# Performance work log

Measured on AMD Instinct MI355X. Metric: run time of the kernel, lower is better.

Reference implementation:

```python
import jax, jax.numpy as jnp
import numpy as np

_BN_EPS = 1e-5
_BN_SCALE = 1.0 / np.sqrt(1.0 + _BN_EPS)  # eval-mode BN with running_mean=0, running_var=1


def _bn(x, g, b):
    # eval-mode BatchNorm1d over channel dim (last axis here)
    return x * (g * _BN_SCALE) + b


def _sa_layer(src_xyz, dst_xyz, cur_i, idx, empty, p_w, p_g, p_b, m_w, m_g, m_b):
    # src_xyz: (N,3), dst_xyz: (M,3), cur_i: (N,D), idx: (M,S) int, empty: (M,) bool
    idx = idx.astype(jnp.int32)
    sp = src_xyz[idx]                       # (M,S,3) neighbor gather
    dp = dst_xyz[:, None, :]                # (M,1,3)
    feat6 = jnp.concatenate([sp - dp, jnp.broadcast_to(dp, sp.shape)], axis=-1)  # (M,S,6)
    off = jax.nn.silu(_bn(jnp.einsum('msc,dc->msd', feat6, p_w), p_g, p_b))      # (M,S,D)
    x = off + cur_i[idx]                    # (M,S,D)
    x = jnp.where(empty[:, None, None], 0.0, x)
    h = jax.nn.relu(_bn(jnp.einsum('msd,hd->msh', x, m_w), m_g, m_b))            # (M,S,H)
    return jnp.max(h, axis=1)               # (M,H) max-pool over neighbors


def reference(src_xyz, src_feats, dst_xyz, idx0, idx1, empty0, empty1,
              fc0_w, fc0_b, p0_w, p0_g, p0_b, m0_w, m0_g, m0_b,
              fc1_w, fc1_b, p1_w, p1_g, p1_b, m1_w, m1_g, m1_b,
              out_w, out_g, out_b):
    cur0 = src_feats @ fc0_w.T + fc0_b      # (N,64) fc_i of layer 0
    cur1 = src_feats @ fc1_w.T + fc1_b      # (N,64) fc_i of layer 1
    f0 = _sa_layer(src_xyz, dst_xyz, cur0, idx0, empty0, p0_w, p0_g, p0_b, m0_w, m0_g, m0_b)
    f1 = _sa_layer(src_xyz, dst_xyz, cur1, idx1, empty1, p1_w, p1_g, p1_b, m1_w, m1_g, m1_b)
    feats = jnp.concatenate([f0, f1], axis=1)                                    # (M,256)
    out = jax.nn.relu(_bn(feats @ out_w.T, out_g, out_b))                        # out_conv (1x1 conv)
    return out                               # (M,256)


def setup_inputs() -> dict:
    key = jax.random.key(0)
    ks = jax.random.split(key, 24)
    N, M, Cin, D, H, S0, S1 = 65536, 16384, 64, 64, 128, 16, 32
    inp = {
        'src_xyz': jax.random.normal(ks[0], (N, 3), jnp.float32) * 20.0,
        'src_feats': jax.random.normal(ks[1], (N, Cin), jnp.float32),
        'dst_xyz': jax.random.normal(ks[2], (M, 3), jnp.float32) * 20.0,
        'idx0': jax.random.randint(ks[3], (M, S0), 0, N, jnp.int32),
        'idx1': jax.random.randint(ks[4], (M, S1), 0, N, jnp.int32),
        'empty0': jax.random.bernoulli(ks[5], 0.05, (M,)),
        'empty1': jax.random.bernoulli(ks[6], 0.05, (M,)),
        'fc0_w': jax.random.normal(ks[7], (D, Cin), jnp.float32) / np.sqrt(Cin),
        'fc0_b': jnp.zeros((D,), jnp.float32),
        'p0_w': jax.random.normal(ks[8], (D, 6), jnp.float32) / np.sqrt(6.0),
        'p0_g': jnp.ones((D,), jnp.float32),
        'p0_b': jnp.zeros((D,), jnp.float32),
        'm0_w': jax.random.normal(ks[9], (H, D), jnp.float32) / np.sqrt(D),
        'm0_g': jnp.ones((H,), jnp.float32),
        'm0_b': jnp.zeros((H,), jnp.float32),
        'fc1_w': jax.random.normal(ks[10], (D, Cin), jnp.float32) / np.sqrt(Cin),
        'fc1_b': jnp.zeros((D,), jnp.float32),
        'p1_w': jax.random.normal(ks[11], (D, 6), jnp.float32) / np.sqrt(6.0),
        'p1_g': jnp.ones((D,), jnp.float32),
        'p1_b': jnp.zeros((D,), jnp.float32),
        'm1_w': jax.random.normal(ks[12], (H, D), jnp.float32) / np.sqrt(D),
        'm1_g': jnp.ones((H,), jnp.float32),
        'm1_b': jnp.zeros((H,), jnp.float32),
        'out_w': jax.random.normal(ks[13], (256, 2 * H), jnp.float32) / np.sqrt(2.0 * H),
        'out_g': jnp.ones((256,), jnp.float32),
        'out_b': jnp.zeros((256,), jnp.float32),
    }
    return inp
```

## Files before the change

kernel.cpp:

```cpp
#include <hip/hip_runtime.h>
#include <hip/hip_bf16.h>

typedef unsigned short ushort_t;
typedef unsigned int uint_t;
typedef __attribute__((ext_vector_type(8))) short v8s;
typedef __attribute__((ext_vector_type(4))) float v4f;

#define BN_SCALE 0.9999950000374997f

__device__ __forceinline__ float bf2f(ushort_t u) {
    union { uint_t i; float f; } v;
    v.i = ((uint_t)u) << 16;
    return v.f;
}
__device__ __forceinline__ ushort_t f2bf(float f) {
    union { uint_t i; float f; } v;
    v.f = f;
    uint_t b = v.i;
    b += 0x7fffu + ((b >> 16) & 1u);
    return (ushort_t)(b >> 16);
}

__device__ __forceinline__ v8s cvt8(const float* __restrict__ p) {
    v8s f;
    #pragma unroll
    for (int j = 0; j < 8; ++j) f[j] = (short)f2bf(p[j]);
    return f;
}

__global__ __launch_bounds__(256) void convw_kernel(
    const float* __restrict__ w, ushort_t* __restrict__ wb)
{
    const int i = (blockIdx.x * 256 + threadIdx.x) * 4;
    const v4f v = *(const v4f*)(w + i);
    ushort_t r0 = f2bf(v[0]), r1 = f2bf(v[1]), r2 = f2bf(v[2]), r3 = f2bf(v[3]);
    uint_t lo = (uint_t)r0 | ((uint_t)r1 << 16);
    uint_t hi = (uint_t)r2 | ((uint_t)r3 << 16);
    *(uint2*)(wb + i) = make_uint2(lo, hi);
}

__global__ __launch_bounds__(256) void cur_kernel(
    const float* __restrict__ src_feats,
    const float* __restrict__ fc0_w, const float* __restrict__ fc0_b,
    const float* __restrict__ fc1_w, const float* __restrict__ fc1_b,
    ushort_t* __restrict__ cur0, ushort_t* __restrict__ cur1)
{
    const int tid  = threadIdx.x;
    const int lane = tid & 63;
    const int wid  = tid >> 6;
    const int col  = lane & 15;
    const int quad = lane >> 4;
    const int row0 = blockIdx.x * 64 + wid * 16;

    v8s afrag[2];
    #pragma unroll
    for (int kf = 0; kf < 2; ++kf)
        afrag[kf] = cvt8(src_feats + (size_t)(row0 + col) * 64 + kf * 32 + quad * 8);

    v4f acc[8];
    v8s bfrag[8][2];
    #pragma unroll
    for (int ct = 0; ct < 8; ++ct) {
        const int d = (ct & 3) * 16 + col;
        const float* w = (ct < 4 ? fc0_w : fc1_w) + d * 64;
        const float  b = (ct < 4 ? fc0_b : fc1_b)[d];
        acc[ct] = (v4f){b, b, b, b};
        #pragma unroll
        for (int kf = 0; kf < 2; ++kf)
            bfrag[ct][kf] = cvt8(w + kf * 32 + quad * 8);
    }

    #pragma unroll
    for (int kf = 0; kf < 2; ++kf)
        #pragma unroll
        for (int ct = 0; ct < 8; ++ct)
            acc[ct] = __builtin_amdgcn_mfma_f32_16x16x32_bf16(
                afrag[kf], bfrag[ct][kf], acc[ct], 0, 0, 0);

    #pragma unroll
    for (int ct = 0; ct < 8; ++ct) {
        ushort_t* dst = (ct < 4) ? cur0 : cur1;
        const int d = (ct & 3) * 16 + col;
        #pragma unroll
        for (int r = 0; r < 4; ++r) {
            const int n = row0 + quad * 4 + r;
            dst[(size_t)n * 64 + d] = f2bf(acc[ct][r]);
        }
    }
}

template <int S>
__device__ __forceinline__ void sa_body(
    const int bid,
    const float* __restrict__ src_xyz,
    const float* __restrict__ dst_xyz,
    const int*   __restrict__ idx,
    const int*   __restrict__ empty,
    const float* __restrict__ p_w,
    const float* __restrict__ p_g,
    const float* __restrict__ p_b,
    const float* __restrict__ m_w,
    const float* __restrict__ m_g,
    const float* __restrict__ m_b,
    const ushort_t* __restrict__ cur,
    ushort_t*    __restrict__ f01,
    const int layer_off,
    ushort_t* xlds,
    v4f*      flds)
{
    constexpr int PAIRS = 128;
    constexpr int MB = PAIRS / S;
    constexpr int XP = 72;
    constexpr int T  = S / 4;

    const int tid  = threadIdx.x;
    const int lane = tid & 63;
    const int wid  = tid >> 6;
    const int m0   = bid * MB;

    {
        const int p  = tid >> 1;
        const int hf = tid & 1;
        const int m  = m0 + p / S;
        const int i  = idx[(size_t)m * S + (p & (S - 1))];
        const uint_t* crow = (const uint_t*)(cur + (size_t)i * 64) + hf * 16;
        const uint4 c0 = *(const uint4*)(crow + 0);
        const uint4 c1 = *(const uint4*)(crow + 4);
        const uint4 c2 = *(const uint4*)(crow + 8);
        const uint4 c3 = *(const uint4*)(crow + 12);
        uint_t* drow = (uint_t*)(xlds + p * XP) + hf * 16;
        *(uint4*)(drow + 0)  = c0;
        *(uint4*)(drow + 4)  = c1;
        *(uint4*)(drow + 8)  = c2;
        *(uint4*)(drow + 12) = c3;
    }
    if (tid < PAIRS) {
        const int p = tid;
        const int m = m0 + p / S;
        const int i = idx[(size_t)m * S + (p & (S - 1))];
        const float dx = dst_xyz[m * 3 + 0];
        const float dy = dst_xyz[m * 3 + 1];
        const float dz = dst_xyz[m * 3 + 2];
        v4f r;
        r[0] = src_xyz[i * 3 + 0] - dx;
        r[1] = src_xyz[i * 3 + 1] - dy;
        r[2] = src_xyz[i * 3 + 2] - dz;
        r[3] = 0.0f;
        flds[p] = r;
    }

    const int dd = (lane & 31) * 2;
    const int psub = lane >> 5;
    const float pgA = p_g[dd] * BN_SCALE;
    const float pgB = p_g[dd + 1] * BN_SCALE;
    const float pbA = p_b[dd];
    const float pbB = p_b[dd + 1];
    const float pwA0 = p_w[dd * 6 + 0] * pgA;
    const float pwA1 = p_w[dd * 6 + 1] * pgA;
    const float pwA2 = p_w[dd * 6 + 2] * pgA;
    const float pdA0 = p_w[dd * 6 + 3] * pgA;
    const float pdA1 = p_w[dd * 6 + 4] * pgA;
    const float pdA2 = p_w[dd * 6 + 5] * pgA;
    const float pwB0 = p_w[dd * 6 + 6] * pgB;
    const float pwB1 = p_w[dd * 6 + 7] * pgB;
    const float pwB2 = p_w[dd * 6 + 8] * pgB;
    const float pdB0 = p_w[dd * 6 + 9] * pgB;
    const float pdB1 = p_w[dd * 6 + 10] * pgB;
    const float pdB2 = p_w[dd * 6 + 11] * pgB;

    __syncthreads();

    const int tbase = wid * T;
    #pragma unroll
    for (int mi = 0; mi < MB; ++mi) {
        const int m = m0 + mi;
        const float dx = dst_xyz[m * 3 + 0];
        const float dy = dst_xyz[m * 3 + 1];
        const float dz = dst_xyz[m * 3 + 2];
        const int   em = empty[m];
        const float vbA = fmaf(pdA0, dx, fmaf(pdA1, dy, fmaf(pdA2, dz, pbA)));
        const float vbB = fmaf(pdB0, dx, fmaf(pdB1, dy, fmaf(pdB2, dz, pbB)));

        #pragma unroll
        for (int it = 0; it < T / 2; ++it) {
            const int p = mi * S + tbase + it * 2 + psub;
            const v4f r = flds[p];
            const uint_t cu = *(const uint_t*)(xlds + p * XP + dd);
            const float c0 = __uint_as_float(cu << 16);
            const float c1 = __uint_as_float(cu & 0xffff0000u);

            const float v0 = fmaf(pwA0, r[0], fmaf(pwA1, r[1], fmaf(pwA2, r[2], vbA)));
            const float v1 = fmaf(pwB0, r[0], fmaf(pwB1, r[1], fmaf(pwB2, r[2], vbB)));
            const float rc0 = __builtin_amdgcn_rcpf(1.0f + __expf(-v0));
            const float rc1 = __builtin_amdgcn_rcpf(1.0f + __expf(-v1));
            float x0 = fmaf(v0, rc0, c0);
            float x1 = fmaf(v1, rc1, c1);
            x0 = em ? 0.0f : x0;
            x1 = em ? 0.0f : x1;

            float2 f2; f2.x = x0; f2.y = x1;
            union { __hip_bfloat162 h2; uint_t u; } pk;
            pk.h2 = __float22bfloat162_rn(f2);
            *(uint_t*)(xlds + p * XP + dd) = pk.u;
        }
    }

    const int col  = lane & 15;
    const int quad = lane >> 4;
    v8s bfrag[2][2];
    float mgv[2], mbv[2];
    #pragma unroll
    for (int c = 0; c < 2; ++c) {
        const int h = (wid * 2 + c) * 16 + col;
        #pragma unroll
        for (int kf = 0; kf < 2; ++kf)
            bfrag[c][kf] = cvt8(m_w + h * 64 + kf * 32 + quad * 8);
        mgv[c] = m_g[h] * BN_SCALE;
        mbv[c] = m_b[h];
    }

    __syncthreads();

    #pragma unroll
    for (int mi = 0; mi < MB; ++mi) {
        const int m = m0 + mi;
        v4f acc[S / 16][2];
        #pragma unroll
        for (int rt = 0; rt < S / 16; ++rt)
            #pragma unroll
            for (int c = 0; c < 2; ++c)
                acc[rt][c] = (v4f)0.0f;

        #pragma unroll
        for (int rt = 0; rt < S / 16; ++rt) {
            #pragma unroll
            for (int kf = 0; kf < 2; ++kf) {
                const v8s afrag = *(const v8s*)(
                    xlds + ((mi * S + rt * 16 + col)) * XP + kf * 32 + quad * 8);
                acc[rt][0] = __builtin_amdgcn_mfma_f32_16x16x32_bf16(
                    afrag, bfrag[0][kf], acc[rt][0], 0, 0, 0);
                acc[rt][1] = __builtin_amdgcn_mfma_f32_16x16x32_bf16(
                    afrag, bfrag[1][kf], acc[rt][1], 0, 0, 0);
            }
        }

        float vmax0 = 0.0f, vmax1 = 0.0f;
        #pragma unroll
        for (int c = 0; c < 2; ++c) {
            float vm = 0.0f;
            #pragma unroll
            for (int rt = 0; rt < S / 16; ++rt)
                #pragma unroll
                for (int r = 0; r < 4; ++r) {
                    const float y = fmaf(acc[rt][c][r], mgv[c], mbv[c]);
                    vm = fmaxf(vm, y);
                }
            vm = fmaxf(vm, __shfl_xor(vm, 16));
            vm = fmaxf(vm, __shfl_xor(vm, 32));
            if (c == 0) vmax0 = vm; else vmax1 = vm;
        }
        if (lane < 32) {
            const int c = lane >> 4;
            const float val = (c == 0) ? vmax0 : vmax1;
            f01[m * 256 + layer_off + (wid * 2 + c) * 16 + (lane & 15)] = f2bf(val);
        }
    }
}

__global__ __launch_bounds__(256, 6) void sa_fused_kernel(
    const float* __restrict__ src_xyz, const float* __restrict__ dst_xyz,
    const int* __restrict__ idx0, const int* __restrict__ empty0,
    const float* __restrict__ p0_w, const float* __restrict__ p0_g, const float* __restrict__ p0_b,
    const float* __restrict__ m0_w, const float* __restrict__ m0_g, const float* __restrict__ m0_b,
    const ushort_t* __restrict__ cur0,
    const int* __restrict__ idx1, const int* __restrict__ empty1,
    const float* __restrict__ p1_w, const float* __restrict__ p1_g, const float* __restrict__ p1_b,
    const float* __restrict__ m1_w, const float* __restrict__ m1_g, const float* __restrict__ m1_b,
    const ushort_t* __restrict__ cur1,
    ushort_t* __restrict__ f01, const int G32)
{
    __shared__ ushort_t xlds[128 * 72];
    __shared__ v4f      flds[128];

    const int b = blockIdx.x;
    if (b < G32)
        sa_body<32>(b, src_xyz, dst_xyz, idx1, empty1, p1_w, p1_g, p1_b,
                    m1_w, m1_g, m1_b, cur1, f01, 128, xlds, flds);
    else
        sa_body<16>(b - G32, src_xyz, dst_xyz, idx0, empty0, p0_w, p0_g, p0_b,
                    m0_w, m0_g, m0_b, cur0, f01, 0, xlds, flds);
}

__global__ __launch_bounds__(256) void out_kernel(
    const ushort_t* __restrict__ f01,
    const ushort_t* __restrict__ out_wb,
    const float*    __restrict__ out_g,
    const float*    __restrict__ out_b,
    float*          __restrict__ out)
{
    const int tid  = threadIdx.x;
    const int lane = tid & 63;
    const int wid  = tid >> 6;
    const int col  = lane & 15;
    const int quad = lane >> 4;
    const int m0   = blockIdx.x * 16;

    v8s afrag[8];
    #pragma unroll
    for (int kf = 0; kf < 8; ++kf)
        afrag[kf] = *(const v8s*)(f01 + (size_t)(m0 + col) * 256 + kf * 32 + quad * 8);

    v4f acc[4];
    #pragma unroll
    for (int c = 0; c < 4; ++c) acc[c] = (v4f)0.0f;

    #pragma unroll
    for (int kf = 0; kf < 8; ++kf) {
        #pragma unroll
        for (int c = 0; c < 4; ++c) {
            const int n = (wid * 4 + c) * 16 + col;
            const v8s b = *(const v8s*)(out_wb + (size_t)n * 256 + kf * 32 + quad * 8);
            acc[c] = __builtin_amdgcn_mfma_f32_16x16x32_bf16(afrag[kf], b, acc[c], 0, 0, 0);
        }
    }

    #pragma unroll
    for (int c = 0; c < 4; ++c) {
        const int n  = (wid * 4 + c) * 16 + col;
        const float og = out_g[n] * BN_SCALE;
        const float ob = out_b[n];
        #pragma unroll
        for (int r = 0; r < 4; ++r) {
            float y = fmaf(acc[c][r], og, ob);
            y = fmaxf(y, 0.0f);
            out[(size_t)(m0 + quad * 4 + r) * 256 + n] = y;
        }
    }
}

extern "C" void kernel_launch(void* const* d_in, const int* in_sizes, int n_in,
                              void* d_out, int out_size, void* d_ws, size_t ws_size,
                              hipStream_t stream)
{
    const float* src_xyz   = (const float*)d_in[0];
    const float* src_feats = (const float*)d_in[1];
    const float* dst_xyz   = (const float*)d_in[2];
    const int*   idx0      = (const int*)d_in[3];
    const int*   idx1      = (const int*)d_in[4];
    const int*   empty0    = (const int*)d_in[5];
    const int*   empty1    = (const int*)d_in[6];
    const float* fc0_w     = (const float*)d_in[7];
    const float* fc0_b     = (const float*)d_in[8];
    const float* p0_w      = (const float*)d_in[9];
    const float* p0_g      = (const float*)d_in[10];
    const float* p0_b      = (const float*)d_in[11];
    const float* m0_w      = (const float*)d_in[12];
    const float* m0_g      = (const float*)d_in[13];
    const float* m0_b      = (const float*)d_in[14];
    const float* fc1_w     = (const float*)d_in[15];
    const float* fc1_b     = (const float*)d_in[16];
    const float* p1_w      = (const float*)d_in[17];
    const float* p1_g      = (const float*)d_in[18];
    const float* p1_b      = (const float*)d_in[19];
    const float* m1_w      = (const float*)d_in[20];
    const float* m1_g      = (const float*)d_in[21];
    const float* m1_b      = (const float*)d_in[22];
    const float* out_w     = (const float*)d_in[23];
    const float* out_g     = (const float*)d_in[24];
    const float* out_b     = (const float*)d_in[25];

    const int N = in_sizes[0] / 3;
    const int M = in_sizes[2] / 3;

    ushort_t* cur0   = (ushort_t*)d_ws;
    ushort_t* cur1   = cur0 + (size_t)N * 64;
    ushort_t* f01    = cur1 + (size_t)N * 64;
    ushort_t* out_wb = f01 + (size_t)M * 256;

    const int G32 = M / 4;
    const int G16 = M / 8;

    convw_kernel<<<64, 256, 0, stream>>>(out_w, out_wb);
    cur_kernel<<<N / 64, 256, 0, stream>>>(src_feats, fc0_w, fc0_b, fc1_w, fc1_b,
                                           cur0, cur1);
    sa_fused_kernel<<<G32 + G16, 256, 0, stream>>>(
        src_xyz, dst_xyz,
        idx0, empty0, p0_w, p0_g, p0_b, m0_w, m0_g, m0_b, cur0,
        idx1, empty1, p1_w, p1_g, p1_b, m1_w, m1_g, m1_b, cur1,
        f01, G32);
    out_kernel<<<M / 16, 256, 0, stream>>>(f01, out_wb, out_g, out_b,
                                           (float*)d_out);
}
```

Baseline: 202.6 us.

## Split MLP work by neighbor-group per wave and pre-convert m_w to bf16

The MFMA stage changes from each wave handling 32 output channels for every centroid to each wave owning whole centroids and computing all 128 channels. A-fragments are loaded from LDS once per centroid and reused across 8 channel tiles. B-fragments now come from a bf16 weight copy produced by extra convw launches instead of per-thread fp32-to-bf16 conversion. This cuts redundant LDS A reads and conversion work, but adds per-iteration global/L1 weight loads, two small extra launches, and lowers the occupancy hint from 6 to 5.

```diff
diff --git a/kernel.cpp b/kernel.cpp
--- a/kernel.cpp
+++ b/kernel.cpp
@@ -99,7 +99,7 @@
     const float* __restrict__ p_w,
     const float* __restrict__ p_g,
     const float* __restrict__ p_b,
-    const float* __restrict__ m_w,
+    const ushort_t* __restrict__ m_wb,
     const float* __restrict__ m_g,
     const float* __restrict__ m_b,
     const ushort_t* __restrict__ cur,
@@ -112,6 +112,8 @@
     constexpr int MB = PAIRS / S;
     constexpr int XP = 72;
     constexpr int T  = S / 4;
+    constexpr int RT = S / 16;
+    constexpr int MW = MB / 4;
 
     const int tid  = threadIdx.x;
     const int lane = tid & 63;
@@ -207,75 +209,70 @@
 
     const int col  = lane & 15;
     const int quad = lane >> 4;
-    v8s bfrag[2][2];
-    float mgv[2], mbv[2];
-    #pragma unroll
-    for (int c = 0; c < 2; ++c) {
-        const int h = (wid * 2 + c) * 16 + col;
-        #pragma unroll
-        for (int kf = 0; kf < 2; ++kf)
-            bfrag[c][kf] = cvt8(m_w + h * 64 + kf * 32 + quad * 8);
-        mgv[c] = m_g[h] * BN_SCALE;
-        mbv[c] = m_b[h];
+    float mgv[8], mbv[8];
+    #pragma unroll
+    for (int ct = 0; ct < 8; ++ct) {
+        const int h = ct * 16 + col;
+        mgv[ct] = m_g[h] * BN_SCALE;
+        mbv[ct] = m_b[h];
     }
 
     __syncthreads();
 
     #pragma unroll
-    for (int mi = 0; mi < MB; ++mi) {
-        const int m = m0 + mi;
-        v4f acc[S / 16][2];
-        #pragma unroll
-        for (int rt = 0; rt < S / 16; ++rt)
+    for (int mw = 0; mw < MW; ++mw) {
+        const int mi = wid + mw * 4;
+        const int m  = m0 + mi;
+
+        v8s afrag[RT][2];
+        #pragma unroll
+        for (int rt = 0; rt < RT; ++rt)
             #pragma unroll
-            for (int c = 0; c < 2; ++c)
-                acc[rt][c] = (v4f)0.0f;
-
-        #pragma unroll
-        for (int rt = 0; rt < S / 16; ++rt) {
+            for (int kf = 0; kf < 2; ++kf)
+                afrag[rt][kf] = *(const v8s*)(
+                    xlds + (mi * S + rt * 16 + col) * XP + kf * 32 + quad * 8);
+
+        #pragma unroll
+        for (int ct = 0; ct < 8; ++ct) {
+            const int h = ct * 16 + col;
+            v4f acc[RT];
+            #pragma unroll
+            for (int rt = 0; rt < RT; ++rt) acc[rt] = (v4f)0.0f;
+
             #pragma unroll
             for (int kf = 0; kf < 2; ++kf) {
-                const v8s afrag = *(const v8s*)(
-                    xlds + ((mi * S + rt * 16 + col)) * XP + kf * 32 + quad * 8);
-                acc[rt][0] = __builtin_amdgcn_mfma_f32_16x16x32_bf16(
-                    afrag, bfrag[0][kf], acc[rt][0], 0, 0, 0);
-                acc[rt][1] = __builtin_amdgcn_mfma_f32_16x16x32_bf16(
-                    afrag, bfrag[1][kf], acc[rt][1], 0, 0, 0);
+                const v8s bfrag = *(const v8s*)(m_wb + h * 64 + kf * 32 + quad * 8);
+                #pragma unroll
+                for (int rt = 0; rt < RT; ++rt)
+                    acc[rt] = __builtin_amdgcn_mfma_f32_16x16x32_bf16(
+                        afrag[rt][kf], bfrag, acc[rt], 0, 0, 0);
             }
-        }
-
-        float vmax0 = 0.0f, vmax1 = 0.0f;
-        #pragma unroll
-        for (int c = 0; c < 2; ++c) {
+
             float vm = 0.0f;
             #pragma unroll
-            for (int rt = 0; rt < S / 16; ++rt)
+            for (int rt = 0; rt < RT; ++rt)
                 #pragma unroll
                 for (int r = 0; r < 4; ++r) {
-                    const float y = fmaf(acc[rt][c][r], mgv[c], mbv[c]);
+                    const float y = fmaf(acc[rt][r], mgv[ct], mbv[ct]);
                     vm = fmaxf(vm, y);
                 }
             vm = fmaxf(vm, __shfl_xor(vm, 16));
             vm = fmaxf(vm, __shfl_xor(vm, 32));
-            if (c == 0) vmax0 = vm; else vmax1 = vm;
-        }
-        if (lane < 32) {
-            const int c = lane >> 4;
-            const float val = (c == 0) ? vmax0 : vmax1;
-            f01[m * 256 + layer_off + (wid * 2 + c) * 16 + (lane & 15)] = f2bf(val);
-        }
-    }
-}
-
-__global__ __launch_bounds__(256, 6) void sa_fused_kernel(
+            if (lane < 16)
+                f01[m * 256 + layer_off + ct * 16 + lane] = f2bf(vm);
+        }
+    }
+}
+
+__global__ __launch_bounds__(256, 5) void sa_fused_kernel(
     const float* __restrict__ src_xyz, const float* __restrict__ dst_xyz,
     const int* __restrict__ idx0, const int* __restrict__ empty0,
     const float* __restrict__ p0_w, const float* __restrict__ p0_g, const float* __restrict__ p0_b,
-    const float* __restrict__ m0_w, const float* __restrict__ m0_g, const float* __restrict__ m0_b,
+    const ushort_t* __restrict__ m0_wb, const float* __restrict__ m0_g, const float* __restrict__ m0_b,
     const ushort_t* __restrict__ cur0,
     const int* __restrict__ idx1, const int* __restrict__ empty1,
     const float* __restrict__ p1_w, const float* __restrict__ p1_g, const float* __restrict__ p1_b,
-    const float* __restrict__ m1_w, const float* __restrict__ m1_g, const float* __restrict__ m1_b,
+    const ushort_t* __restrict__ m1_wb, const float* __restrict__ m1_g, const float* __restrict__ m1_b,
     const ushort_t* __restrict__ cur1,
     ushort_t* __restrict__ f01, const int G32)
 {
@@ -285,10 +282,10 @@
     const int b = blockIdx.x;
     if (b < G32)
         sa_body<32>(b, src_xyz, dst_xyz, idx1, empty1, p1_w, p1_g, p1_b,
-                    m1_w, m1_g, m1_b, cur1, f01, 128, xlds, flds);
+                    m1_wb, m1_g, m1_b, cur1, f01, 128, xlds, flds);
     else
         sa_body<16>(b - G32, src_xyz, dst_xyz, idx0, empty0, p0_w, p0_g, p0_b,
-                    m0_w, m0_g, m0_b, cur0, f01, 0, xlds, flds);
+                    m0_wb, m0_g, m0_b, cur0, f01, 0, xlds, flds);
 }
 
 __global__ __launch_bounds__(256) void out_kernel(
@@ -376,17 +373,21 @@
     ushort_t* cur1   = cur0 + (size_t)N * 64;
     ushort_t* f01    = cur1 + (size_t)N * 64;
     ushort_t* out_wb = f01 + (size_t)M * 256;
+    ushort_t* m0_wb  = out_wb + 256 * 256;
+    ushort_t* m1_wb  = m0_wb + 128 * 64;
 
     const int G32 = M / 4;
     const int G16 = M / 8;
 
     convw_kernel<<<64, 256, 0, stream>>>(out_w, out_wb);
+    convw_kernel<<<8, 256, 0, stream>>>(m0_w, m0_wb);
+    convw_kernel<<<8, 256, 0, stream>>>(m1_w, m1_wb);
     cur_kernel<<<N / 64, 256, 0, stream>>>(src_feats, fc0_w, fc0_b, fc1_w, fc1_b,
                                            cur0, cur1);
     sa_fused_kernel<<<G32 + G16, 256, 0, stream>>>(
         src_xyz, dst_xyz,
-        idx0, empty0, p0_w, p0_g, p0_b, m0_w, m0_g, m0_b, cur0,
-        idx1, empty1, p1_w, p1_g, p1_b, m1_w, m1_g, m1_b, cur1,
+        idx0, empty0, p0_w, p0_g, p0_b, m0_wb, m0_g, m0_b, cur0,
+        idx1, empty1, p1_w, p1_g, p1_b, m1_wb, m1_g, m1_b, cur1,
         f01, G32);
     out_kernel<<<M / 16, 256, 0, stream>>>(f01, out_wb, out_g, out_b,
                                            (float*)d_out);
```

Measured after the change: 225.4 us. +11.3%, slower.
